# Performance work log

Hardware: AMD Instinct MI355X
Metric: run time of the kernel (lower is better)

## Reference

```python
import jax, jax.numpy as jnp
import numpy as np
from jax import lax


def avg_pool3(x):
    # F.avg_pool2d(x, 3, 1, 1) with count_include_pad=True: zero-pad, divide by 9.
    s = lax.reduce_window(x, 0.0, lax.add, (1, 1, 3, 3), (1, 1, 1, 1),
                          [(0, 0), (0, 0), (1, 1), (1, 1)])
    return s / 9.0


def resize_bilinear_ac(x, H, W):
    # bilinear resize with align_corners=True, separable gathers
    B, C, h, w = x.shape
    if (h, w) == (H, W):
        return x
    yc = jnp.linspace(0.0, h - 1.0, H)
    xc = jnp.linspace(0.0, w - 1.0, W)
    y0 = jnp.floor(yc).astype(jnp.int32); y1 = jnp.minimum(y0 + 1, h - 1)
    x0 = jnp.floor(xc).astype(jnp.int32); x1 = jnp.minimum(x0 + 1, w - 1)
    wy = (yc - y0).astype(x.dtype)
    wx = (xc - x0).astype(x.dtype)
    xr = x[:, :, y0, :] * (1.0 - wy)[None, None, :, None] + x[:, :, y1, :] * wy[None, None, :, None]
    return xr[:, :, :, x0] * (1.0 - wx) + xr[:, :, :, x1] * wx


def grid_sample_border(img, grid):
    # F.grid_sample(mode='bilinear', padding_mode='border', align_corners=True)
    B, C, H, W = img.shape
    x = jnp.clip((grid[..., 0] + 1.0) * 0.5 * (W - 1), 0.0, W - 1.0)
    y = jnp.clip((grid[..., 1] + 1.0) * 0.5 * (H - 1), 0.0, H - 1.0)
    x0 = jnp.floor(x).astype(jnp.int32); y0 = jnp.floor(y).astype(jnp.int32)
    x1 = jnp.minimum(x0 + 1, W - 1); y1 = jnp.minimum(y0 + 1, H - 1)
    wx = (x - x0)[..., None]; wy = (y - y0)[..., None]
    imt = jnp.transpose(img, (0, 2, 3, 1))  # [B,H,W,C]
    b = jnp.arange(B)[:, None, None]
    v00 = imt[b, y0, x0]; v01 = imt[b, y0, x1]
    v10 = imt[b, y1, x0]; v11 = imt[b, y1, x1]
    top = v00 * (1.0 - wx) + v01 * wx
    bot = v10 * (1.0 - wx) + v11 * wx
    out = top * (1.0 - wy) + bot * wy
    return jnp.transpose(out, (0, 3, 1, 2))


def warp_image(img, flow):
    B, C, H, W = img.shape
    _, _, h, w = flow.shape
    flow = resize_bilinear_ac(flow, H, W)
    scale = jnp.array([W / w, H / h], dtype=img.dtype).reshape(1, 2, 1, 1)
    flow = flow * scale
    yy, xx = jnp.meshgrid(jnp.linspace(-1.0, 1.0, H, dtype=img.dtype),
                          jnp.linspace(-1.0, 1.0, W, dtype=img.dtype), indexing='ij')
    base = jnp.stack((xx, yy), axis=-1)[None]  # [1,H,W,2]
    fn = jnp.stack([2.0 * flow[:, 0] / max(W - 1, 1),
                    2.0 * flow[:, 1] / max(H - 1, 1)], axis=-1)  # [B,H,W,2]
    return grid_sample_border(img, base + fn)


def ssim_map(x, y, C1=0.01 ** 2, C2=0.03 ** 2):
    mu_x = avg_pool3(x); mu_y = avg_pool3(y)
    sigma_x = avg_pool3(x * x) - mu_x * mu_x
    sigma_y = avg_pool3(y * y) - mu_y * mu_y
    sigma_xy = avg_pool3(x * y) - mu_x * mu_y
    ssim = (2 * mu_x * mu_y + C1) * (2 * sigma_xy + C2) / \
           ((mu_x ** 2 + mu_y ** 2 + C1) * (sigma_x + sigma_y + C2) + 1e-12)
    return jnp.mean(jnp.clip((1.0 - ssim) / 2.0, 0.0, 1.0), axis=1, keepdims=True)


def masked_mean(x, mask):
    m = (mask > 0.5).astype(x.dtype)
    num = jnp.sum(x * m)
    den = jnp.maximum(jnp.sum(m), 1.0)
    return num / den


def smoothness_loss(flow):
    dx = jnp.abs(flow[:, :, :, :-1] - flow[:, :, :, 1:])
    dy = jnp.abs(flow[:, :, :-1, :] - flow[:, :, 1:, :])
    return jnp.mean(dx) + jnp.mean(dy)


def setup_inputs() -> dict:
    key = jax.random.key(0)
    k1, k2, k3, k4 = jax.random.split(key, 4)
    B, H, W = 8, 512, 1024
    h, w = 128, 256
    return {
        'flow': jax.random.normal(k1, (B, 2, h, w), dtype=jnp.float32),
        'img1': jax.random.uniform(k2, (B, 3, H, W), dtype=jnp.float32),
        'img2': jax.random.uniform(k3, (B, 3, H, W), dtype=jnp.float32),
        'valid_mask': jax.random.uniform(k4, (B, 1, H, W), dtype=jnp.float32),
    }


def reference(flow, img1, img2, valid_mask):
    alpha_photo, alpha_smooth = 1.0, 0.1
    img2_warp = warp_image(img2, flow)
    l1 = jnp.mean(jnp.abs(img1 - img2_warp), axis=1, keepdims=True)
    photo_map = 0.85 * ssim_map(img1, img2_warp) + 0.15 * l1
    photo = masked_mean(photo_map, valid_mask)
    smooth = smoothness_loss(flow)
    total = alpha_photo * photo + alpha_smooth * smooth
    return (total, photo, smooth)
```

## Files before the change

### kernel.cpp

```cpp
#include <hip/hip_runtime.h>
#include <hip/hip_fp16.h>

#define B_   8
#define H_   512
#define W_   1024
#define FH_  128
#define FW_  256
#define TW   64
#define TH   16
#define HW_  (TW + 2)
#define HH_  (TH + 2)
#define NHALO (HH_ * HW_)
#define FR_  8
#define FC_  20
#define NSLOT 256

__device__ __forceinline__ float wave_reduce(float v) {
    #pragma unroll
    for (int off = 32; off > 0; off >>= 1) v += __shfl_down(v, off, 64);
    return v;
}

__device__ __forceinline__ void hrow(const __half2* __restrict__ s,
                                     float& hA, float& hB, float& hAA, float& hBB, float& hAB) {
    const float2 p0 = __half22float2(s[0]);
    const float2 p1 = __half22float2(s[1]);
    const float2 p2 = __half22float2(s[2]);
    hA  = p0.x + p1.x + p2.x;
    hB  = p0.y + p1.y + p2.y;
    hAA = fmaf(p0.x, p0.x, fmaf(p1.x, p1.x, p2.x * p2.x));
    hBB = fmaf(p0.y, p0.y, fmaf(p1.y, p1.y, p2.y * p2.y));
    hAB = fmaf(p0.x, p0.y, fmaf(p1.x, p1.y, p2.x * p2.y));
}

__global__ __launch_bounds__(256, 5)
void fused_main(const float* __restrict__ flow, const float* __restrict__ img1,
                const float* __restrict__ img2, const float* __restrict__ mask,
                float* __restrict__ accum) {
    const int bid = blockIdx.x;
    const int lin = (bid & 7) * 512 + (bid >> 3);
    const int b   = lin >> 9;
    const int rem = lin & 511;
    const int ty0 = (rem >> 4) * TH;
    const int tx0 = (rem & 15) * TW;
    const int tid = threadIdx.x;

    __shared__ __half2 sP[3][HH_][HW_];
    __shared__ float   sF[2][FR_][FC_];

    const uint32_t plane = (uint32_t)H_ * W_;
    const float* f0  = flow + (size_t)b * 2 * FH_ * FW_;
    const float* f1  = f0 + FH_ * FW_;
    const float* i10 = img1 + (size_t)b * 3 * plane;
    const float* i11 = i10 + plane;
    const float* i12 = i11 + plane;
    const float* i20 = img2 + (size_t)b * 3 * plane;
    const float* i21 = i20 + plane;
    const float* i22 = i21 + plane;

    const int fx0s = (tx0 > 0) ? (int)((float)(tx0 - 1) * (255.0f / 1023.0f)) : 0;
    const int fy0s = (ty0 > 0) ? (int)((float)(ty0 - 1) * (127.0f / 511.0f)) : 0;
    if (tid < 2 * FR_ * FC_ - 256 || tid < 256) {
    }
    for (int i = tid; i < 2 * FR_ * FC_; i += 256) {
        const int ch = i / (FR_ * FC_);
        const int r  = (i - ch * FR_ * FC_) / FC_;
        const int cc = i - ch * FR_ * FC_ - r * FC_;
        const int sy = min(fy0s + r, FH_ - 1);
        const int sx = min(fx0s + cc, FW_ - 1);
        const float* fp = ch ? f1 : f0;
        sF[ch][r][cc] = fp[(uint32_t)sy * FW_ + (uint32_t)sx];
    }

    const int lx  = tid & 63;
    const int lyg = tid >> 6;
    const int rb  = lyg * 4;
    const float* mb = mask + (size_t)b * plane;
    const uint32_t mb0 = (uint32_t)(ty0 + rb) * W_ + (uint32_t)(tx0 + lx);
    float mreg[4];
    #pragma unroll
    for (int k = 0; k < 4; ++k) mreg[k] = mb[mb0 + (uint32_t)k * W_];

    __syncthreads();

    #pragma unroll
    for (int s = 0; s < 5; ++s) {
        const int i = tid + s * 256;
        if (i < NHALO) {
            const int ly = i / HW_;
            const int lxh = i - ly * HW_;
            const int gy = ty0 + ly - 1;
            const int gx = tx0 + lxh - 1;
            float v10 = 0.f, v11 = 0.f, v12 = 0.f;
            float v20 = 0.f, v21 = 0.f, v22 = 0.f;
            if (gy >= 0 && gy < H_ && gx >= 0 && gx < W_) {
                const uint32_t p = (uint32_t)gy * W_ + (uint32_t)gx;
                v10 = i10[p]; v11 = i11[p]; v12 = i12[p];

                const float yc = gy * (127.0f / 511.0f);
                const float xc = gx * (255.0f / 1023.0f);
                const int y0 = (int)yc, x0 = (int)xc;
                const float wy = yc - (float)y0, wx = xc - (float)x0;
                const int yr = y0 - fy0s, xr = x0 - fx0s;
                const float a00 = sF[0][yr][xr],     a01 = sF[0][yr][xr + 1];
                const float a10 = sF[0][yr + 1][xr], a11 = sF[0][yr + 1][xr + 1];
                const float c00 = sF[1][yr][xr],     c01 = sF[1][yr][xr + 1];
                const float c10 = sF[1][yr + 1][xr], c11 = sF[1][yr + 1][xr + 1];
                const float fxt = a00 + wx * (a01 - a00);
                const float fxb = a10 + wx * (a11 - a10);
                const float fx  = fxt + wy * (fxb - fxt);
                const float fyt = c00 + wx * (c01 - c00);
                const float fyb = c10 + wx * (c11 - c10);
                const float fy  = fyt + wy * (fyb - fyt);

                const float gxs = fminf(fmaxf(fmaf(4.0f, fx, (float)gx), 0.0f), (float)(W_ - 1));
                const float gys = fminf(fmaxf(fmaf(4.0f, fy, (float)gy), 0.0f), (float)(H_ - 1));
                const int sx0 = (int)gxs, sy0 = (int)gys;
                const int sx1 = min(sx0 + 1, W_ - 1);
                const int sy1 = min(sy0 + 1, H_ - 1);
                const float swx = gxs - (float)sx0, swy = gys - (float)sy0;
                const uint32_t p00 = (uint32_t)sy0 * W_ + (uint32_t)sx0;
                const uint32_t p01 = (uint32_t)sy0 * W_ + (uint32_t)sx1;
                const uint32_t p10 = (uint32_t)sy1 * W_ + (uint32_t)sx0;
                const uint32_t p11 = (uint32_t)sy1 * W_ + (uint32_t)sx1;
                {
                    const float t = i20[p00] + swx * (i20[p01] - i20[p00]);
                    const float u = i20[p10] + swx * (i20[p11] - i20[p10]);
                    v20 = t + swy * (u - t);
                }
                {
                    const float t = i21[p00] + swx * (i21[p01] - i21[p00]);
                    const float u = i21[p10] + swx * (i21[p11] - i21[p10]);
                    v21 = t + swy * (u - t);
                }
                {
                    const float t = i22[p00] + swx * (i22[p01] - i22[p00]);
                    const float u = i22[p10] + swx * (i22[p11] - i22[p10]);
                    v22 = t + swy * (u - t);
                }
            }
            sP[0][ly][lxh] = __floats2half2_rn(v10, v20);
            sP[1][ly][lxh] = __floats2half2_rn(v11, v21);
            sP[2][ly][lxh] = __floats2half2_rn(v12, v22);
        }
    }

    __syncthreads();

    const float inv9 = 1.0f / 9.0f;
    const float C1 = 0.0001f, C2 = 0.0009f;
    float dist[4] = {0.f, 0.f, 0.f, 0.f};
    float l1s [4] = {0.f, 0.f, 0.f, 0.f};

    #pragma unroll
    for (int c = 0; c < 3; ++c) {
        float hA0,hB0,hAA0,hBB0,hAB0;
        float hA1,hB1,hAA1,hBB1,hAB1;
        float hA2,hB2,hAA2,hBB2,hAB2;
        hrow(&sP[c][rb + 0][lx], hA0,hB0,hAA0,hBB0,hAB0);
        hrow(&sP[c][rb + 1][lx], hA1,hB1,hAA1,hBB1,hAB1);
        #pragma unroll
        for (int k = 0; k < 4; ++k) {
            hrow(&sP[c][rb + k + 2][lx], hA2,hB2,hAA2,hBB2,hAB2);
            const float sA  = hA0  + hA1  + hA2;
            const float sB  = hB0  + hB1  + hB2;
            const float sAA = hAA0 + hAA1 + hAA2;
            const float sBB = hBB0 + hBB1 + hBB2;
            const float sAB = hAB0 + hAB1 + hAB2;
            const float mx  = sA * inv9, my = sB * inv9;
            const float vx  = fmaf(-mx, mx, sAA * inv9);
            const float vy  = fmaf(-my, my, sBB * inv9);
            const float vxy = fmaf(-mx, my, sAB * inv9);
            const float numt = (2.f * mx * my + C1) * (2.f * vxy + C2);
            const float dent = fmaf(fmaf(mx, mx, fmaf(my, my, C1)), (vx + vy + C2), 1e-12f);
            const float ssim = numt * __builtin_amdgcn_rcpf(dent);
            dist[k] += fminf(fmaxf((1.0f - ssim) * 0.5f, 0.f), 1.f);
            const float2 ctr = __half22float2(sP[c][rb + k + 1][lx + 1]);
            l1s[k] += fabsf(ctr.x - ctr.y);
            hA0 = hA1; hB0 = hB1; hAA0 = hAA1; hBB0 = hBB1; hAB0 = hAB1;
            hA1 = hA2; hB1 = hB2; hAA1 = hAA2; hBB1 = hBB2; hAB1 = hAB2;
        }
    }

    float num_acc = 0.f, den_acc = 0.f;
    #pragma unroll
    for (int k = 0; k < 4; ++k) {
        const float pmv = 0.28333334f * dist[k] + 0.05f * l1s[k];
        const float m   = (mreg[k] > 0.5f) ? 1.f : 0.f;
        num_acc = fmaf(pmv, m, num_acc);
        den_acc += m;
    }

    float num = wave_reduce(num_acc);
    float den = wave_reduce(den_acc);
    __shared__ float rn[4], rd[4];
    const int wid = tid >> 6, lane = tid & 63;
    if (lane == 0) { rn[wid] = num; rd[wid] = den; }
    __syncthreads();
    if (tid == 0) {
        float* slot = accum + (size_t)(bid & (NSLOT - 1)) * 4;
        atomicAdd(&slot[0], rn[0] + rn[1] + rn[2] + rn[3]);
        atomicAdd(&slot[1], rd[0] + rd[1] + rd[2] + rd[3]);
    }
}

__global__ __launch_bounds__(256)
void smooth_kernel(const float* __restrict__ flow, float* __restrict__ accum) {
    const int N = B_ * 2 * FH_ * FW_;
    float dxs = 0.f, dys = 0.f;
    for (int i = blockIdx.x * 256 + threadIdx.x; i < N; i += gridDim.x * 256) {
        const float f = flow[i];
        const int x = i & (FW_ - 1);
        const int y = (i >> 8) & (FH_ - 1);
        if (x < FW_ - 1) dxs += fabsf(f - flow[i + 1]);
        if (y < FH_ - 1) dys += fabsf(f - flow[i + FW_]);
    }
    dxs = wave_reduce(dxs);
    dys = wave_reduce(dys);
    __shared__ float rn[4], rd[4];
    const int wid = threadIdx.x >> 6, lane = threadIdx.x & 63;
    if (lane == 0) { rn[wid] = dxs; rd[wid] = dys; }
    __syncthreads();
    if (threadIdx.x == 0) {
        float* slot = accum + (size_t)blockIdx.x * 4;
        atomicAdd(&slot[2], rn[0] + rn[1] + rn[2] + rn[3]);
        atomicAdd(&slot[3], rd[0] + rd[1] + rd[2] + rd[3]);
    }
}

__global__ __launch_bounds__(256)
void finalize_kernel(const float* __restrict__ accum, float* __restrict__ out) {
    const int t = threadIdx.x;
    float num = accum[t * 4 + 0];
    float den = accum[t * 4 + 1];
    float dxs = accum[t * 4 + 2];
    float dys = accum[t * 4 + 3];
    num = wave_reduce(num); den = wave_reduce(den);
    dxs = wave_reduce(dxs); dys = wave_reduce(dys);
    __shared__ float r[4][4];
    const int wid = t >> 6, lane = t & 63;
    if (lane == 0) { r[wid][0] = num; r[wid][1] = den; r[wid][2] = dxs; r[wid][3] = dys; }
    __syncthreads();
    if (t == 0) {
        const float tn = r[0][0] + r[1][0] + r[2][0] + r[3][0];
        const float td = r[0][1] + r[1][1] + r[2][1] + r[3][1];
        const float tx = r[0][2] + r[1][2] + r[2][2] + r[3][2];
        const float ty = r[0][3] + r[1][3] + r[2][3] + r[3][3];
        const float photo   = tn / fmaxf(td, 1.0f);
        const float mean_dx = tx / (float)(B_ * 2 * FH_ * (FW_ - 1));
        const float mean_dy = ty / (float)(B_ * 2 * (FH_ - 1) * FW_);
        const float smooth  = mean_dx + mean_dy;
        out[0] = photo + 0.1f * smooth;
        out[1] = photo;
        out[2] = smooth;
    }
}

extern "C" void kernel_launch(void* const* d_in, const int* in_sizes, int n_in,
                              void* d_out, int out_size, void* d_ws, size_t ws_size,
                              hipStream_t stream) {
    const float* flow = (const float*)d_in[0];
    const float* img1 = (const float*)d_in[1];
    const float* img2 = (const float*)d_in[2];
    const float* mask = (const float*)d_in[3];
    float* out   = (float*)d_out;
    float* accum = (float*)d_ws;

    hipMemsetAsync(accum, 0, NSLOT * 4 * sizeof(float), stream);
    smooth_kernel<<<NSLOT, 256, 0, stream>>>(flow, accum);
    fused_main<<<(W_ / TW) * (H_ / TH) * B_, 256, 0, stream>>>(flow, img1, img2, mask, accum);
    finalize_kernel<<<1, 256, 0, stream>>>(accum, out);
}
```

Baseline: 196.0 us.

## Batch halo gather loads two slots at a time with branchless clamped addressing

Splits the halo fill into an issue phase that clamps coordinates and issues all 15 gather loads per slot unconditionally, and a commit phase that interpolates and masks out-of-bounds results. Two slots are issued before either is committed, so more global loads are in flight per thread and memory latency can overlap. Occupancy is lowered from 5 to 4 waves per SIMD via launch_bounds to leave room for the extra live registers. Border and tail pixels now perform redundant clamped loads instead of branching around them.

```diff
diff --git a/kernel.cpp b/kernel.cpp
--- a/kernel.cpp
+++ b/kernel.cpp
@@ -33,7 +33,17 @@
     hAB = fmaf(p0.x, p0.y, fmaf(p1.x, p1.y, p2.x * p2.y));
 }
 
-__global__ __launch_bounds__(256, 5)
+struct Taps {
+    float a0, a1, a2;
+    float r00, r01, r10, r11;
+    float g00, g01, g10, g11;
+    float b00, b01, b10, b11;
+    float swx, swy;
+    int   ly, lxh;
+    bool  inb;
+};
+
+__global__ __launch_bounds__(256, 4)
 void fused_main(const float* __restrict__ flow, const float* __restrict__ img1,
                 const float* __restrict__ img2, const float* __restrict__ mask,
                 float* __restrict__ accum) {
@@ -60,8 +70,6 @@
 
     const int fx0s = (tx0 > 0) ? (int)((float)(tx0 - 1) * (255.0f / 1023.0f)) : 0;
     const int fy0s = (ty0 > 0) ? (int)((float)(ty0 - 1) * (127.0f / 511.0f)) : 0;
-    if (tid < 2 * FR_ * FC_ - 256 || tid < 256) {
-    }
     for (int i = tid; i < 2 * FR_ * FC_; i += 256) {
         const int ch = i / (FR_ * FC_);
         const int r  = (i - ch * FR_ * FC_) / FC_;
@@ -83,66 +91,83 @@
 
     __syncthreads();
 
-    #pragma unroll
-    for (int s = 0; s < 5; ++s) {
-        const int i = tid + s * 256;
-        if (i < NHALO) {
-            const int ly = i / HW_;
-            const int lxh = i - ly * HW_;
-            const int gy = ty0 + ly - 1;
-            const int gx = tx0 + lxh - 1;
-            float v10 = 0.f, v11 = 0.f, v12 = 0.f;
-            float v20 = 0.f, v21 = 0.f, v22 = 0.f;
-            if (gy >= 0 && gy < H_ && gx >= 0 && gx < W_) {
-                const uint32_t p = (uint32_t)gy * W_ + (uint32_t)gx;
-                v10 = i10[p]; v11 = i11[p]; v12 = i12[p];
-
-                const float yc = gy * (127.0f / 511.0f);
-                const float xc = gx * (255.0f / 1023.0f);
-                const int y0 = (int)yc, x0 = (int)xc;
-                const float wy = yc - (float)y0, wx = xc - (float)x0;
-                const int yr = y0 - fy0s, xr = x0 - fx0s;
-                const float a00 = sF[0][yr][xr],     a01 = sF[0][yr][xr + 1];
-                const float a10 = sF[0][yr + 1][xr], a11 = sF[0][yr + 1][xr + 1];
-                const float c00 = sF[1][yr][xr],     c01 = sF[1][yr][xr + 1];
-                const float c10 = sF[1][yr + 1][xr], c11 = sF[1][yr + 1][xr + 1];
-                const float fxt = a00 + wx * (a01 - a00);
-                const float fxb = a10 + wx * (a11 - a10);
-                const float fx  = fxt + wy * (fxb - fxt);
-                const float fyt = c00 + wx * (c01 - c00);
-                const float fyb = c10 + wx * (c11 - c10);
-                const float fy  = fyt + wy * (fyb - fyt);
-
-                const float gxs = fminf(fmaxf(fmaf(4.0f, fx, (float)gx), 0.0f), (float)(W_ - 1));
-                const float gys = fminf(fmaxf(fmaf(4.0f, fy, (float)gy), 0.0f), (float)(H_ - 1));
-                const int sx0 = (int)gxs, sy0 = (int)gys;
-                const int sx1 = min(sx0 + 1, W_ - 1);
-                const int sy1 = min(sy0 + 1, H_ - 1);
-                const float swx = gxs - (float)sx0, swy = gys - (float)sy0;
-                const uint32_t p00 = (uint32_t)sy0 * W_ + (uint32_t)sx0;
-                const uint32_t p01 = (uint32_t)sy0 * W_ + (uint32_t)sx1;
-                const uint32_t p10 = (uint32_t)sy1 * W_ + (uint32_t)sx0;
-                const uint32_t p11 = (uint32_t)sy1 * W_ + (uint32_t)sx1;
-                {
-                    const float t = i20[p00] + swx * (i20[p01] - i20[p00]);
-                    const float u = i20[p10] + swx * (i20[p11] - i20[p10]);
-                    v20 = t + swy * (u - t);
-                }
-                {
-                    const float t = i21[p00] + swx * (i21[p01] - i21[p00]);
-                    const float u = i21[p10] + swx * (i21[p11] - i21[p10]);
-                    v21 = t + swy * (u - t);
-                }
-                {
-                    const float t = i22[p00] + swx * (i22[p01] - i22[p00]);
-                    const float u = i22[p10] + swx * (i22[p11] - i22[p10]);
-                    v22 = t + swy * (u - t);
-                }
-            }
-            sP[0][ly][lxh] = __floats2half2_rn(v10, v20);
-            sP[1][ly][lxh] = __floats2half2_rn(v11, v21);
-            sP[2][ly][lxh] = __floats2half2_rn(v12, v22);
+    auto issue_slot = [&](int s) -> Taps {
+        Taps t;
+        const int iraw = tid + s * 256;
+        const int i  = min(iraw, NHALO - 1);
+        const int ly = i / HW_;
+        const int lxh = i - ly * HW_;
+        const int gy = ty0 + ly - 1;
+        const int gx = tx0 + lxh - 1;
+        t.ly = ly; t.lxh = lxh;
+        t.inb = (gy >= 0 && gy < H_ && gx >= 0 && gx < W_);
+        const int gyc = min(max(gy, 0), H_ - 1);
+        const int gxc = min(max(gx, 0), W_ - 1);
+        const uint32_t p = (uint32_t)gyc * W_ + (uint32_t)gxc;
+
+        const float yc = gyc * (127.0f / 511.0f);
+        const float xc = gxc * (255.0f / 1023.0f);
+        const int y0 = (int)yc, x0 = (int)xc;
+        const float wy = yc - (float)y0, wx = xc - (float)x0;
+        const int yr = y0 - fy0s, xr = x0 - fx0s;
+        const float a00 = sF[0][yr][xr],     a01 = sF[0][yr][xr + 1];
+        const float a10 = sF[0][yr + 1][xr], a11 = sF[0][yr + 1][xr + 1];
+        const float c00 = sF[1][yr][xr],     c01 = sF[1][yr][xr + 1];
+        const float c10 = sF[1][yr + 1][xr], c11 = sF[1][yr + 1][xr + 1];
+        const float fxt = fmaf(wx, a01 - a00, a00);
+        const float fxb = fmaf(wx, a11 - a10, a10);
+        const float fx  = fmaf(wy, fxb - fxt, fxt);
+        const float fyt = fmaf(wx, c01 - c00, c00);
+        const float fyb = fmaf(wx, c11 - c10, c10);
+        const float fy  = fmaf(wy, fyb - fyt, fyt);
+
+        const float gxs = fminf(fmaxf(fmaf(4.0f, fx, (float)gxc), 0.0f), (float)(W_ - 1));
+        const float gys = fminf(fmaxf(fmaf(4.0f, fy, (float)gyc), 0.0f), (float)(H_ - 1));
+        const int sx0 = (int)gxs, sy0 = (int)gys;
+        const int dx = (sx0 < W_ - 1) ? 1 : 0;
+        const int dyw = (sy0 < H_ - 1) ? W_ : 0;
+        t.swx = gxs - (float)sx0;
+        t.swy = gys - (float)sy0;
+        const uint32_t p00 = (uint32_t)sy0 * W_ + (uint32_t)sx0;
+        const uint32_t p01 = p00 + dx;
+        const uint32_t p10 = p00 + dyw;
+        const uint32_t p11 = p00 + dyw + dx;
+
+        t.a0  = i10[p];   t.a1  = i11[p];   t.a2  = i12[p];
+        t.r00 = i20[p00]; t.r01 = i20[p01]; t.r10 = i20[p10]; t.r11 = i20[p11];
+        t.g00 = i21[p00]; t.g01 = i21[p01]; t.g10 = i21[p10]; t.g11 = i21[p11];
+        t.b00 = i22[p00]; t.b01 = i22[p01]; t.b10 = i22[p10]; t.b11 = i22[p11];
+        return t;
+    };
+
+    auto commit_slot = [&](const Taps& t, int s) {
+        const float rt = fmaf(t.swx, t.r01 - t.r00, t.r00);
+        const float rbt = fmaf(t.swx, t.r11 - t.r10, t.r10);
+        const float v20 = fmaf(t.swy, rbt - rt, rt);
+        const float gt = fmaf(t.swx, t.g01 - t.g00, t.g00);
+        const float gbt = fmaf(t.swx, t.g11 - t.g10, t.g10);
+        const float v21 = fmaf(t.swy, gbt - gt, gt);
+        const float bt = fmaf(t.swx, t.b01 - t.b00, t.b00);
+        const float bbt = fmaf(t.swx, t.b11 - t.b10, t.b10);
+        const float v22 = fmaf(t.swy, bbt - bt, bt);
+        const float z = t.inb ? 1.0f : 0.0f;
+        const bool wr = (s < 4) || (tid + s * 256 < NHALO);
+        if (wr) {
+            sP[0][t.ly][t.lxh] = __floats2half2_rn(t.a0 * z, v20 * z);
+            sP[1][t.ly][t.lxh] = __floats2half2_rn(t.a1 * z, v21 * z);
+            sP[2][t.ly][t.lxh] = __floats2half2_rn(t.a2 * z, v22 * z);
         }
+    };
+
+    {
+        Taps t0 = issue_slot(0);
+        Taps t1 = issue_slot(1);
+        commit_slot(t0, 0); commit_slot(t1, 1);
+        Taps t2 = issue_slot(2);
+        Taps t3 = issue_slot(3);
+        commit_slot(t2, 2); commit_slot(t3, 3);
+        Taps t4 = issue_slot(4);
+        commit_slot(t4, 4);
     }
 
     __syncthreads();
```

Result: slower. 207.0 us (+5.6%).

## Pack img2 into interleaved half-precision RGB for the warp gather

Applied to the files above, without the earlier changes.

Adds a pre-pass that converts img2 from planar fp32 into an interleaved 8-byte half4 layout, so each bilinear tap in the warp needs one 8-byte load instead of three scattered fp32 loads. The fused kernel also raises its occupancy hint to 8 waves, turns the unrolled halo loop into a strided loop and uses explicit fma in the lerps. The packed path is used only when the workspace holds about 33 MB, and it adds an extra full read of img2 and a write of the packed copy on every call. Sampling warped values from fp16 loses precision, although those values were already stored as fp16 in shared memory before.

```diff
diff --git a/kernel.cpp b/kernel.cpp
--- a/kernel.cpp
+++ b/kernel.cpp
@@ -14,6 +14,9 @@
 #define FR_  8
 #define FC_  20
 #define NSLOT 256
+#define PLANE (H_ * W_)
+
+struct alignas(8) H4 { __half2 a; __half2 b; };
 
 __device__ __forceinline__ float wave_reduce(float v) {
     #pragma unroll
@@ -33,10 +36,30 @@
     hAB = fmaf(p0.x, p0.y, fmaf(p1.x, p1.y, p2.x * p2.y));
 }
 
-__global__ __launch_bounds__(256, 5)
+__global__ __launch_bounds__(256)
+void pack_img2(const float* __restrict__ img2, H4* __restrict__ pk) {
+    const int total = B_ * PLANE;
+    const int stride = gridDim.x * 256 * 4;
+    for (int base = (blockIdx.x * 256 + threadIdx.x) * 4; base < total; base += stride) {
+        const int b = base >> 19;
+        const int p = base & (PLANE - 1);
+        const float* pr = img2 + (size_t)b * 3 * PLANE;
+        const float4 r  = *(const float4*)&pr[p];
+        const float4 g  = *(const float4*)&pr[p + PLANE];
+        const float4 bl = *(const float4*)&pr[p + 2 * PLANE];
+        H4* o = pk + (size_t)b * PLANE + p;
+        o[0] = { __floats2half2_rn(r.x, g.x), __floats2half2_rn(bl.x, 0.f) };
+        o[1] = { __floats2half2_rn(r.y, g.y), __floats2half2_rn(bl.y, 0.f) };
+        o[2] = { __floats2half2_rn(r.z, g.z), __floats2half2_rn(bl.z, 0.f) };
+        o[3] = { __floats2half2_rn(r.w, g.w), __floats2half2_rn(bl.w, 0.f) };
+    }
+}
+
+template <int PK>
+__global__ __launch_bounds__(256, 8)
 void fused_main(const float* __restrict__ flow, const float* __restrict__ img1,
                 const float* __restrict__ img2, const float* __restrict__ mask,
-                float* __restrict__ accum) {
+                const H4* __restrict__ pk, float* __restrict__ accum) {
     const int bid = blockIdx.x;
     const int lin = (bid & 7) * 512 + (bid >> 3);
     const int b   = lin >> 9;
@@ -48,20 +71,18 @@
     __shared__ __half2 sP[3][HH_][HW_];
     __shared__ float   sF[2][FR_][FC_];
 
-    const uint32_t plane = (uint32_t)H_ * W_;
     const float* f0  = flow + (size_t)b * 2 * FH_ * FW_;
     const float* f1  = f0 + FH_ * FW_;
-    const float* i10 = img1 + (size_t)b * 3 * plane;
-    const float* i11 = i10 + plane;
-    const float* i12 = i11 + plane;
-    const float* i20 = img2 + (size_t)b * 3 * plane;
-    const float* i21 = i20 + plane;
-    const float* i22 = i21 + plane;
+    const float* i10 = img1 + (size_t)b * 3 * PLANE;
+    const float* i11 = i10 + PLANE;
+    const float* i12 = i11 + PLANE;
+    const float* i20 = img2 + (size_t)b * 3 * PLANE;
+    const float* i21 = i20 + PLANE;
+    const float* i22 = i21 + PLANE;
+    const H4*    pkb = pk + (size_t)b * PLANE;
 
     const int fx0s = (tx0 > 0) ? (int)((float)(tx0 - 1) * (255.0f / 1023.0f)) : 0;
     const int fy0s = (ty0 > 0) ? (int)((float)(ty0 - 1) * (127.0f / 511.0f)) : 0;
-    if (tid < 2 * FR_ * FC_ - 256 || tid < 256) {
-    }
     for (int i = tid; i < 2 * FR_ * FC_; i += 256) {
         const int ch = i / (FR_ * FC_);
         const int r  = (i - ch * FR_ * FC_) / FC_;
@@ -75,7 +96,7 @@
     const int lx  = tid & 63;
     const int lyg = tid >> 6;
     const int rb  = lyg * 4;
-    const float* mb = mask + (size_t)b * plane;
+    const float* mb = mask + (size_t)b * PLANE;
     const uint32_t mb0 = (uint32_t)(ty0 + rb) * W_ + (uint32_t)(tx0 + lx);
     float mreg[4];
     #pragma unroll
@@ -83,66 +104,86 @@
 
     __syncthreads();
 
-    #pragma unroll
-    for (int s = 0; s < 5; ++s) {
-        const int i = tid + s * 256;
-        if (i < NHALO) {
-            const int ly = i / HW_;
-            const int lxh = i - ly * HW_;
-            const int gy = ty0 + ly - 1;
-            const int gx = tx0 + lxh - 1;
-            float v10 = 0.f, v11 = 0.f, v12 = 0.f;
-            float v20 = 0.f, v21 = 0.f, v22 = 0.f;
-            if (gy >= 0 && gy < H_ && gx >= 0 && gx < W_) {
-                const uint32_t p = (uint32_t)gy * W_ + (uint32_t)gx;
-                v10 = i10[p]; v11 = i11[p]; v12 = i12[p];
-
-                const float yc = gy * (127.0f / 511.0f);
-                const float xc = gx * (255.0f / 1023.0f);
-                const int y0 = (int)yc, x0 = (int)xc;
-                const float wy = yc - (float)y0, wx = xc - (float)x0;
-                const int yr = y0 - fy0s, xr = x0 - fx0s;
-                const float a00 = sF[0][yr][xr],     a01 = sF[0][yr][xr + 1];
-                const float a10 = sF[0][yr + 1][xr], a11 = sF[0][yr + 1][xr + 1];
-                const float c00 = sF[1][yr][xr],     c01 = sF[1][yr][xr + 1];
-                const float c10 = sF[1][yr + 1][xr], c11 = sF[1][yr + 1][xr + 1];
-                const float fxt = a00 + wx * (a01 - a00);
-                const float fxb = a10 + wx * (a11 - a10);
-                const float fx  = fxt + wy * (fxb - fxt);
-                const float fyt = c00 + wx * (c01 - c00);
-                const float fyb = c10 + wx * (c11 - c10);
-                const float fy  = fyt + wy * (fyb - fyt);
-
-                const float gxs = fminf(fmaxf(fmaf(4.0f, fx, (float)gx), 0.0f), (float)(W_ - 1));
-                const float gys = fminf(fmaxf(fmaf(4.0f, fy, (float)gy), 0.0f), (float)(H_ - 1));
-                const int sx0 = (int)gxs, sy0 = (int)gys;
-                const int sx1 = min(sx0 + 1, W_ - 1);
-                const int sy1 = min(sy0 + 1, H_ - 1);
-                const float swx = gxs - (float)sx0, swy = gys - (float)sy0;
-                const uint32_t p00 = (uint32_t)sy0 * W_ + (uint32_t)sx0;
-                const uint32_t p01 = (uint32_t)sy0 * W_ + (uint32_t)sx1;
-                const uint32_t p10 = (uint32_t)sy1 * W_ + (uint32_t)sx0;
-                const uint32_t p11 = (uint32_t)sy1 * W_ + (uint32_t)sx1;
-                {
-                    const float t = i20[p00] + swx * (i20[p01] - i20[p00]);
-                    const float u = i20[p10] + swx * (i20[p11] - i20[p10]);
-                    v20 = t + swy * (u - t);
-                }
-                {
-                    const float t = i21[p00] + swx * (i21[p01] - i21[p00]);
-                    const float u = i21[p10] + swx * (i21[p11] - i21[p10]);
-                    v21 = t + swy * (u - t);
-                }
-                {
-                    const float t = i22[p00] + swx * (i22[p01] - i22[p00]);
-                    const float u = i22[p10] + swx * (i22[p11] - i22[p10]);
-                    v22 = t + swy * (u - t);
+    for (int i = tid; i < NHALO; i += 256) {
+        const int ly = i / HW_;
+        const int lxh = i - ly * HW_;
+        const int gy = ty0 + ly - 1;
+        const int gx = tx0 + lxh - 1;
+        float v10 = 0.f, v11 = 0.f, v12 = 0.f;
+        float v20 = 0.f, v21 = 0.f, v22 = 0.f;
+        if (gy >= 0 && gy < H_ && gx >= 0 && gx < W_) {
+            const uint32_t p = (uint32_t)gy * W_ + (uint32_t)gx;
+            v10 = i10[p]; v11 = i11[p]; v12 = i12[p];
+
+            const float yc = gy * (127.0f / 511.0f);
+            const float xc = gx * (255.0f / 1023.0f);
+            const int y0 = (int)yc, x0 = (int)xc;
+            const float wy = yc - (float)y0, wx = xc - (float)x0;
+            const int yr = y0 - fy0s, xr = x0 - fx0s;
+            const float a00 = sF[0][yr][xr],     a01 = sF[0][yr][xr + 1];
+            const float a10 = sF[0][yr + 1][xr], a11 = sF[0][yr + 1][xr + 1];
+            const float c00 = sF[1][yr][xr],     c01 = sF[1][yr][xr + 1];
+            const float c10 = sF[1][yr + 1][xr], c11 = sF[1][yr + 1][xr + 1];
+            const float fxt = fmaf(wx, a01 - a00, a00);
+            const float fxb = fmaf(wx, a11 - a10, a10);
+            const float fx  = fmaf(wy, fxb - fxt, fxt);
+            const float fyt = fmaf(wx, c01 - c00, c00);
+            const float fyb = fmaf(wx, c11 - c10, c10);
+            const float fy  = fmaf(wy, fyb - fyt, fyt);
+
+            const float gxs = fminf(fmaxf(fmaf(4.0f, fx, (float)gx), 0.0f), (float)(W_ - 1));
+            const float gys = fminf(fmaxf(fmaf(4.0f, fy, (float)gy), 0.0f), (float)(H_ - 1));
+            const int sx0 = (int)gxs, sy0 = (int)gys;
+            const int sx1 = min(sx0 + 1, W_ - 1);
+            const int sy1 = min(sy0 + 1, H_ - 1);
+            const float swx = gxs - (float)sx0, swy = gys - (float)sy0;
+            const uint32_t p00 = (uint32_t)sy0 * W_ + (uint32_t)sx0;
+            const uint32_t p01 = (uint32_t)sy0 * W_ + (uint32_t)sx1;
+            const uint32_t p10 = (uint32_t)sy1 * W_ + (uint32_t)sx0;
+            const uint32_t p11 = (uint32_t)sy1 * W_ + (uint32_t)sx1;
+
+            if (PK) {
+                const H4 q00 = pkb[p00], q01 = pkb[p01], q10 = pkb[p10], q11 = pkb[p11];
+                const float2 rg00 = __half22float2(q00.a), rg01 = __half22float2(q01.a);
+                const float2 rg10 = __half22float2(q10.a), rg11 = __half22float2(q11.a);
+                const float b00 = __low2float(q00.b), b01 = __low2float(q01.b);
+                const float b10 = __low2float(q10.b), b11 = __low2float(q11.b);
+                {
+                    const float t = fmaf(swx, rg01.x - rg00.x, rg00.x);
+                    const float u = fmaf(swx, rg11.x - rg10.x, rg10.x);
+                    v20 = fmaf(swy, u - t, t);
+                }
+                {
+                    const float t = fmaf(swx, rg01.y - rg00.y, rg00.y);
+                    const float u = fmaf(swx, rg11.y - rg10.y, rg10.y);
+                    v21 = fmaf(swy, u - t, t);
+                }
+                {
+                    const float t = fmaf(swx, b01 - b00, b00);
+                    const float u = fmaf(swx, b11 - b10, b10);
+                    v22 = fmaf(swy, u - t, t);
+                }
+            } else {
+                {
+                    const float t = fmaf(swx, i20[p01] - i20[p00], i20[p00]);
+                    const float u = fmaf(swx, i20[p11] - i20[p10], i20[p10]);
+                    v20 = fmaf(swy, u - t, t);
+                }
+                {
+                    const float t = fmaf(swx, i21[p01] - i21[p00], i21[p00]);
+                    const float u = fmaf(swx, i21[p11] - i21[p10], i21[p10]);
+                    v21 = fmaf(swy, u - t, t);
+                }
+                {
+                    const float t = fmaf(swx, i22[p01] - i22[p00], i22[p00]);
+                    const float u = fmaf(swx, i22[p11] - i22[p10], i22[p10]);
+                    v22 = fmaf(swy, u - t, t);
                 }
             }
-            sP[0][ly][lxh] = __floats2half2_rn(v10, v20);
-            sP[1][ly][lxh] = __floats2half2_rn(v11, v21);
-            sP[2][ly][lxh] = __floats2half2_rn(v12, v22);
         }
+        sP[0][ly][lxh] = __floats2half2_rn(v10, v20);
+        sP[1][ly][lxh] = __floats2half2_rn(v11, v21);
+        sP[2][ly][lxh] = __floats2half2_rn(v12, v22);
     }
 
     __syncthreads();
@@ -265,9 +306,19 @@
     const float* mask = (const float*)d_in[3];
     float* out   = (float*)d_out;
     float* accum = (float*)d_ws;
+    H4*    pk    = (H4*)((char*)d_ws + 4096);
+
+    const size_t need = 4096 + sizeof(H4) * (size_t)B_ * PLANE;
+    const bool packed = ws_size >= need;
 
     hipMemsetAsync(accum, 0, NSLOT * 4 * sizeof(float), stream);
     smooth_kernel<<<NSLOT, 256, 0, stream>>>(flow, accum);
-    fused_main<<<(W_ / TW) * (H_ / TH) * B_, 256, 0, stream>>>(flow, img1, img2, mask, accum);
+    const int grid = (W_ / TW) * (H_ / TH) * B_;
+    if (packed) {
+        pack_img2<<<2048, 256, 0, stream>>>(img2, pk);
+        fused_main<1><<<grid, 256, 0, stream>>>(flow, img1, img2, mask, pk, accum);
+    } else {
+        fused_main<0><<<grid, 256, 0, stream>>>(flow, img1, img2, mask, pk, accum);
+    }
     finalize_kernel<<<1, 256, 0, stream>>>(accum, out);
 }
```

Measured after the change: 187.9 us. -4.1%, faster.
